# Kernel tuning notes

Hardware: AMD Instinct MI355X
Metric: run time of the kernel (lower is better)

## Reference

```python
import jax, jax.numpy as jnp
import numpy as np

TAU_EPS = 1e-6
T_SCALAR = 1.0  # call() default t when given a single tensor
NUM_HEADS = 8


def setup_inputs() -> dict:
    key = jax.random.key(0)
    ks = jax.random.split(key, 12)
    B, T, dm = 4, 1024, 512
    ph, th = 64, 32  # phi hidden, tau hidden
    pd = 128         # 2 * depth (pairwise concat dim per head)

    def w(k, shape):
        return jax.random.normal(k, shape, jnp.float32) / jnp.sqrt(jnp.float32(shape[0]))

    return {
        "x": jax.random.normal(ks[0], (B, T, dm), jnp.float32),
        "Wq": w(ks[1], (dm, dm)), "bq": jnp.zeros((dm,), jnp.float32),
        "Wk": w(ks[2], (dm, dm)), "bk": jnp.zeros((dm,), jnp.float32),
        "Wv": w(ks[3], (dm, dm)), "bv": jnp.zeros((dm,), jnp.float32),
        "Wphi_in": w(ks[4], (pd, ph)), "bphi_in": jnp.zeros((ph,), jnp.float32),
        "Wphi_out": w(ks[5], (ph, 1)), "bphi_out": jnp.zeros((1,), jnp.float32),
        "Wta": w(ks[6], (pd, 1)), "bta": jnp.zeros((1,), jnp.float32),
        "Wtb": w(ks[7], (pd, 1)), "btb": jnp.zeros((1,), jnp.float32),
        "Wtau_in": w(ks[8], (pd, th)), "btau_in": jnp.zeros((th,), jnp.float32),
        "Wtau_out": w(ks[9], (th, 1)), "btau_out": jnp.zeros((1,), jnp.float32),
        "Wo": w(ks[10], (dm, dm)), "bo": jnp.zeros((dm,), jnp.float32),
    }


def _lan_forward(x, Wq, bq, Wk, bk, Wv, bv,
                 Wphi_in, bphi_in, Wphi_out, bphi_out,
                 Wta, bta, Wtb, btb,
                 Wtau_in, btau_in, Wtau_out, btau_out,
                 Wo, bo):
    B, T, dm = x.shape
    H = NUM_HEADS
    D = dm // H

    def heads(z):  # [B,T,dm] -> [B,H,T,D]
        return z.reshape(B, T, H, D).transpose(0, 2, 1, 3)

    q = heads(x @ Wq + bq)
    k = heads(x @ Wk + bk)
    v = heads(x @ Wv + bv)

    # phi_in/phi_out, tau_in/tau_out, time_a, time_b are all linear Dense
    # layers acting on concat([q_i, k_j]) (dim 2D). A linear map on a concat
    # equals (per-q scalar) + (per-k scalar) + bias, so fold the two-layer
    # linear stacks into a single [2D] vector and broadcast-add -- exact math,
    # no [B,H,T,T,2D] materialization.
    def pair_scalar(w2d, b0):  # w2d: [2D], b0: scalar -> [B,H,Tq,Tk]
        sq = jnp.einsum('bhtd,d->bht', q, w2d[:D])
        sk = jnp.einsum('bhtd,d->bht', k, w2d[D:])
        return sq[..., :, None] + sk[..., None, :] + b0

    w_phi = (Wphi_in @ Wphi_out)[:, 0]
    b_phi = bphi_in @ Wphi_out[:, 0] + bphi_out[0]
    phi = jax.nn.sigmoid(pair_scalar(w_phi, b_phi))

    t_a = pair_scalar(Wta[:, 0], bta[0])
    t_b = pair_scalar(Wtb[:, 0], btb[0])
    t_interp = jax.nn.sigmoid(t_a * T_SCALAR + t_b)

    w_tau = (Wtau_in @ Wtau_out)[:, 0]
    b_tau = btau_in @ Wtau_out[:, 0] + btau_out[0]
    tau = jax.nn.softplus(pair_scalar(w_tau, b_tau)) + TAU_EPS

    # mode == 'exact': a(t) = (phi/tau) * (1 - exp(-tau * t))
    attn_logits = phi / tau * (1.0 - jnp.exp(-tau * t_interp))
    attn = jax.nn.softmax(attn_logits, axis=-1)

    out = jnp.einsum('bhqk,bhkd->bhqd', attn, v)          # [B,H,T,D]
    out = out.transpose(0, 2, 1, 3).reshape(B, T, dm)      # combine heads
    return out @ Wo + bo                                   # return_sequences=True, linear activation


def reference(x, Wq, bq, Wk, bk, Wv, bv,
              Wphi_in, bphi_in, Wphi_out, bphi_out,
              Wta, bta, Wtb, btb,
              Wtau_in, btau_in, Wtau_out, btau_out,
              Wo, bo):
    return _lan_forward(x, Wq, bq, Wk, bk, Wv, bv,
                        Wphi_in, bphi_in, Wphi_out, bphi_out,
                        Wta, bta, Wtb, btb,
                        Wtau_in, btau_in, Wtau_out, btau_out,
                        Wo, bo)
```

## Files before the change

### kernel.cpp

```cpp
#include <hip/hip_runtime.h>
#include <hip/hip_bf16.h>

#define B_  4
#define T_  1024
#define H_  8
#define NTOK (B_*T_)

#define CONST_OFF 512
#define UTH_OFF   576
#define UTL_OFF   12864
#define XHI_OFF   25152
#define WVTH_OFF  2122304
#define WOTH_OFF  2384448
#define S_OFF     2646592
#define VT_OFF    2843200

#define LOG2E 1.4426950408889634f
#define LN2SQ 0.4804530139182014f

typedef __attribute__((ext_vector_type(4))) float v4f;
typedef __attribute__((ext_vector_type(8))) short v8s;

__device__ inline short bf16r(float f) {
  union { float f; unsigned u; } v; v.f = f;
  return (short)((v.u + 0x7FFFu + ((v.u >> 16) & 1u)) >> 16);
}
__device__ inline float bf16f(short s) {
  union { unsigned u; float f; } v; v.u = ((unsigned)(unsigned short)s) << 16; return v.f;
}
__device__ inline unsigned cvt_pk_bf16(float lo, float hi) {
  unsigned r;
  asm("v_cvt_pk_bf16_f32 %0, %1, %2" : "=v"(r) : "v"(lo), "v"(hi));
  return r;
}

__global__ __launch_bounds__(256) void k_prep(
    const float* __restrict__ Wphi_in, const float* __restrict__ Wphi_out,
    const float* __restrict__ bphi_in, const float* __restrict__ bphi_out,
    const float* __restrict__ Wta, const float* __restrict__ bta,
    const float* __restrict__ Wtb, const float* __restrict__ btb,
    const float* __restrict__ Wtau_in, const float* __restrict__ Wtau_out,
    const float* __restrict__ btau_in, const float* __restrict__ btau_out,
    const float* __restrict__ Wq, const float* __restrict__ bq,
    const float* __restrict__ Wk, const float* __restrict__ bk,
    const float* __restrict__ x, const float* __restrict__ Wv, const float* __restrict__ Wo,
    short* __restrict__ Uth, short* __restrict__ Utl, float* __restrict__ consts,
    short* __restrict__ xh,
    short* __restrict__ Wvh, short* __restrict__ Woh) {
  __shared__ float wv[390];
  __shared__ float tile[64][65];
  int bx = blockIdx.x, t = threadIdx.x;
  if (bx < 96) {
    if (t < 128) {
      float wp = 0.f;
      for (int j = 0; j < 64; ++j) wp += Wphi_in[t*64+j] * Wphi_out[j];
      float wt = 0.f;
      for (int j = 0; j < 32; ++j) wt += Wtau_in[t*32+j] * Wtau_out[j];
      wv[t]       = wp;
      wv[128 + t] = Wta[t] + Wtb[t];
      wv[256 + t] = wt;
    } else if (t == 128) {
      float bp = bphi_out[0];
      for (int j = 0; j < 64; ++j) bp += bphi_in[j]*Wphi_out[j];
      float bt = btau_out[0];
      for (int j = 0; j < 32; ++j) bt += btau_in[j]*Wtau_out[j];
      wv[384] = bp;
      wv[385] = bta[0] + btb[0];
      wv[386] = bt;
    }
    __syncthreads();
    int idx = bx*256 + t;
    int c = idx & 511;
    int s = idx >> 9;
    int h = s / 6, tt = s % 6;
    int qk = tt / 3;
    int which = tt % 3;
    float scale = (which == 2) ? LOG2E : -LOG2E;
    const float* W = qk ? Wk : Wq;
    const float* wvec = wv + which*128 + qk*64;
    const float* row = W + c*512 + h*64;
    float acc = 0.f;
    #pragma unroll 8
    for (int d = 0; d < 64; ++d) acc += row[d] * wvec[d];
    float v = acc * scale;
    short hi = bf16r(v);
    Uth[s*512 + c] = hi;
    Utl[s*512 + c] = bf16r(v - bf16f(hi));
    if (c == 0) {
      const float* bb = qk ? bk : bq;
      float cs = 0.f;
      for (int d = 0; d < 64; ++d) cs += bb[h*64+d] * wvec[d];
      if (qk == 0) cs += wv[384 + which];
      consts[s] = cs * scale;
    }
    return;
  }
  if (bx < 1120) {
    size_t i = (size_t)((bx-96)*256 + t) * 8;
    float4 a = *(const float4*)(x + i);
    float4 b = *(const float4*)(x + i + 4);
    float vals[8] = {a.x,a.y,a.z,a.w,b.x,b.y,b.z,b.w};
    v8s hi;
    #pragma unroll
    for (int j = 0; j < 8; ++j) hi[j] = bf16r(vals[j]);
    *(v8s*)(xh + i) = hi;
    return;
  }
  int idx = bx - 1120;
  int z = idx >> 6, rem = idx & 63;
  int k0 = (rem >> 3)*64, n0 = (rem & 7)*64;
  const float* src = z ? Wo : Wv;
  short* dh = z ? Woh : Wvh;
  int kr = t >> 2, cq = t & 3;
  #pragma unroll
  for (int i = 0; i < 4; ++i) {
    float4 v = *(const float4*)(src + (size_t)(k0+kr)*512 + n0 + cq*16 + i*4);
    tile[kr][cq*16+i*4+0] = v.x; tile[kr][cq*16+i*4+1] = v.y;
    tile[kr][cq*16+i*4+2] = v.z; tile[kr][cq*16+i*4+3] = v.w;
  }
  __syncthreads();
  int nr = t >> 2, ko = t & 3;
  v8s h0,h1;
  #pragma unroll
  for (int i = 0; i < 8; ++i) {
    h0[i] = bf16r(tile[ko*16+i][nr]);
    h1[i] = bf16r(tile[ko*16+8+i][nr]);
  }
  size_t base = (size_t)(n0+nr)*512 + k0 + ko*16;
  *(v8s*)(dh + base) = h0; *(v8s*)(dh + base + 8) = h1;
}

template<int MODE>
__device__ __forceinline__ void gemm_body(char* smem, int mb, int nb,
    const short* __restrict__ A, const short* __restrict__ B,
    const float* __restrict__ bias, float* __restrict__ C, short* __restrict__ VT) {
  short (*As)[40] = (short(*)[40])(smem);
  short (*Bs)[40] = (short(*)[40])(smem + 5120);
  int tid = threadIdx.x, l = tid & 63, ra = l & 15, kg = l >> 4;
  int w = tid >> 6, wr = w >> 1, wc = w & 1;
  v4f acc[2][2] = {};
  int srow = tid >> 2, soct = tid & 3;
  const short* gA = A + (size_t)(mb*64+srow)*512 + soct*8;
  const short* gB = B + (size_t)(nb*64+srow)*512 + soct*8;
  v8s sa = *(const v8s*)(gA);
  v8s sc = *(const v8s*)(gB);
  for (int k0 = 0; k0 < 512; k0 += 32) {
    __syncthreads();
    *(v8s*)&As[srow][soct*8] = sa;
    *(v8s*)&Bs[srow][soct*8] = sc;
    if (k0 < 480) {
      sa = *(const v8s*)(gA + k0 + 32);
      sc = *(const v8s*)(gB + k0 + 32);
    }
    __syncthreads();
    v8s a[2], b[2];
    #pragma unroll
    for (int mi = 0; mi < 2; ++mi)
      a[mi] = *(const v8s*)&As[wr*32 + mi*16 + ra][kg*8];
    #pragma unroll
    for (int ni = 0; ni < 2; ++ni)
      b[ni] = *(const v8s*)&Bs[wc*32 + ni*16 + ra][kg*8];
    #pragma unroll
    for (int mi = 0; mi < 2; ++mi)
      #pragma unroll
      for (int ni = 0; ni < 2; ++ni)
        acc[mi][ni] = __builtin_amdgcn_mfma_f32_16x16x32_bf16(a[mi], b[ni], acc[mi][ni], 0, 0, 0);
  }
  if constexpr (MODE == 0) {
    #pragma unroll
    for (int ni = 0; ni < 2; ++ni) {
      int n = nb*64 + wc*32 + ni*16 + ra;
      float bv_ = bias[n];
      #pragma unroll
      for (int mi = 0; mi < 2; ++mi) {
        int row = mb*64 + wr*32 + mi*16 + kg*4;
        #pragma unroll
        for (int r = 0; r < 4; ++r)
          C[(size_t)(row+r)*512 + n] = acc[mi][ni][r] + bv_;
      }
    }
  } else {
    __syncthreads();
    float (*ldsT)[65] = (float(*)[65])(smem);
    #pragma unroll
    for (int ni = 0; ni < 2; ++ni) {
      int lc = wc*32 + ni*16 + ra;
      float bv_ = bias[nb*64 + lc];
      #pragma unroll
      for (int mi = 0; mi < 2; ++mi) {
        int lr = wr*32 + mi*16 + kg*4;
        #pragma unroll
        for (int r = 0; r < 4; ++r)
          ldsT[lc][lr+r] = acc[mi][ni][r] + bv_;
      }
    }
    __syncthreads();
    int d = tid >> 2, tq = tid & 3;
    v8s h0, h1;
    #pragma unroll
    for (int i = 0; i < 8; ++i) {
      h0[i] = bf16r(ldsT[d][tq*16+i]);
      h1[i] = bf16r(ldsT[d][tq*16+8+i]);
    }
    size_t base = ((size_t)(((mb>>4)*8 + nb)*64 + d))*1024 + (mb&15)*64 + tq*16;
    *(v8s*)(VT + base)     = h0;
    *(v8s*)(VT + base + 8) = h1;
  }
}

__device__ __forceinline__ void S_body(char* smem, int mb,
    const short* __restrict__ xh,
    const short* __restrict__ Uth, const short* __restrict__ Utl,
    const float* __restrict__ consts, float* __restrict__ E) {
  float* red = (float*)smem;
  int tid = threadIdx.x, w = tid >> 6, l = tid & 63, ra = l & 15, kg = l >> 4;
  v4f acc[3] = {{0,0,0,0},{0,0,0,0},{0,0,0,0}};
  const short* xa = xh + (size_t)(mb*16+ra)*512;
  #pragma unroll
  for (int ks = 0; ks < 4; ++ks) {
    int kk = w*128 + ks*32 + kg*8;
    v8s ah = *(const v8s*)(xa + kk);
    #pragma unroll
    for (int nf = 0; nf < 3; ++nf) {
      v8s bh = *(const v8s*)(Uth + (size_t)(nf*16+ra)*512 + kk);
      v8s bl = *(const v8s*)(Utl + (size_t)(nf*16+ra)*512 + kk);
      acc[nf] = __builtin_amdgcn_mfma_f32_16x16x32_bf16(ah, bh, acc[nf], 0, 0, 0);
      acc[nf] = __builtin_amdgcn_mfma_f32_16x16x32_bf16(ah, bl, acc[nf], 0, 0, 0);
    }
  }
  if (w > 0) {
    #pragma unroll
    for (int nf = 0; nf < 3; ++nf) *(v4f*)(red + ((w-1)*64 + l)*12 + nf*4) = acc[nf];
  }
  __syncthreads();
  if (w == 0) {
    #pragma unroll
    for (int p = 0; p < 3; ++p)
      #pragma unroll
      for (int nf = 0; nf < 3; ++nf) acc[nf] += *(const v4f*)(red + (p*64 + l)*12 + nf*4);
    int t0 = mb*16 + kg*4;
    #pragma unroll
    for (int nf = 0; nf < 3; ++nf) {
      int s = nf*16 + ra;
      float cns = consts[s];
      v4f o;
      #pragma unroll
      for (int c = 0; c < 4; ++c) o[c] = __builtin_amdgcn_exp2f(acc[nf][c] + cns);
      *(v4f*)(E + (size_t)s*NTOK + t0) = o;
    }
  }
}

__global__ __launch_bounds__(256) void k_mid(
    const short* __restrict__ xh,
    const short* __restrict__ Uth, const short* __restrict__ Utl,
    const float* __restrict__ consts, float* __restrict__ E,
    const short* __restrict__ Wvh,
    const float* __restrict__ bv, short* __restrict__ VT) {
  __shared__ __align__(16) char smem[16640];
  int bx = blockIdx.x;
  if (bx < 256) {
    S_body(smem, bx, xh, Uth, Utl, consts, E);
  } else {
    int i = bx - 256;
    gemm_body<1>(smem, i >> 3, i & 7, xh, Wvh, bv, nullptr, VT);
  }
}

__global__ __launch_bounds__(256) void k_out(
    const short* __restrict__ A, const short* __restrict__ B,
    const float* __restrict__ bias, float* __restrict__ C) {
  __shared__ __align__(16) char smem[16640];
  gemm_body<0>(smem, blockIdx.x, blockIdx.y, A, B, bias, C, nullptr);
}

__global__ __launch_bounds__(256) void k_attn(const float* __restrict__ E,
                                              const short* __restrict__ VT,
                                              short* __restrict__ AOh) {
  __shared__ float red[3][64][40];
  int tid = threadIdx.x, w = tid >> 6, l = tid & 63, ra = l & 15, kg = l >> 4;
  int bh = blockIdx.y, b = bh >> 3, h = bh & 7;
  int q0 = blockIdx.x * 32;
  const float* Eb = E + (size_t)h*6*NTOK + b*T_;
  float eqp[2], eqc[2], eqt[2];
  #pragma unroll
  for (int ai = 0; ai < 2; ++ai) {
    eqp[ai] = Eb[q0 + ai*16 + ra];
    eqc[ai] = Eb[NTOK + q0 + ai*16 + ra];
    eqt[ai] = Eb[2*NTOK + q0 + ai*16 + ra];
  }
  const float* Ekp = Eb + 3*NTOK;
  const float* Ekc = Eb + 4*NTOK;
  const float* Ekt = Eb + 5*NTOK;
  const short* Vb = VT + (size_t)bh*64*1024 + (size_t)ra*1024;

  v4f acc[2][4] = {};
  v4f dacc[2] = {};
  v8s ones;
  #pragma unroll
  for (int j = 0; j < 8; ++j) ones[j] = (short)0x3F80;

  #pragma unroll 2
  for (int ks = 0; ks < 8; ++ks) {
    int kk = w*256 + ks*32 + kg*8;
    v4f p0 = *(const v4f*)&Ekp[kk], p1 = *(const v4f*)&Ekp[kk+4];
    v4f c0 = *(const v4f*)&Ekc[kk], c1 = *(const v4f*)&Ekc[kk+4];
    v4f t0 = *(const v4f*)&Ekt[kk], t1 = *(const v4f*)&Ekt[kk+4];
    v8s bfr[4];
    #pragma unroll
    for (int ni = 0; ni < 4; ++ni) bfr[ni] = *(const v8s*)(Vb + (size_t)ni*16*1024 + kk);
    #pragma unroll
    for (int ai = 0; ai < 2; ++ai) {
      float p8[8];
      #pragma unroll
      for (int j = 0; j < 8; ++j) {
        float Ep = (j < 4) ? p0[j] : p1[j-4];
        float Ec = (j < 4) ? c0[j] : c1[j-4];
        float Et = (j < 4) ? t0[j] : t1[j-4];
        float ephi = eqp[ai] * Ep;
        float ec   = eqc[ai] * Ec;
        float g    = eqt[ai] * Et;
        float ti   = __builtin_amdgcn_rcpf(1.f + ec);
        float t2   = __builtin_amdgcn_logf(1.f + g);
        float z    = 1.f - __builtin_amdgcn_exp2f(-t2 * ti);
        float den  = (1.f + ephi) * fmaf(t2, LN2SQ, 6.93e-7f);
        p8[j] = __builtin_amdgcn_exp2f(z * __builtin_amdgcn_rcpf(den));
      }
      union { unsigned u[4]; v8s s; } af;
      af.u[0] = cvt_pk_bf16(p8[0], p8[1]);
      af.u[1] = cvt_pk_bf16(p8[2], p8[3]);
      af.u[2] = cvt_pk_bf16(p8[4], p8[5]);
      af.u[3] = cvt_pk_bf16(p8[6], p8[7]);
      v8s afrag = af.s;
      #pragma unroll
      for (int ni = 0; ni < 4; ++ni)
        acc[ai][ni] = __builtin_amdgcn_mfma_f32_16x16x32_bf16(afrag, bfr[ni], acc[ai][ni], 0, 0, 0);
      dacc[ai] = __builtin_amdgcn_mfma_f32_16x16x32_bf16(afrag, ones, dacc[ai], 0, 0, 0);
    }
  }

  if (w > 0) {
    float* rp = &red[w-1][l][0];
    #pragma unroll
    for (int ai = 0; ai < 2; ++ai) {
      #pragma unroll
      for (int ni = 0; ni < 4; ++ni) *(v4f*)(rp + ai*16 + ni*4) = acc[ai][ni];
      *(v4f*)(rp + 32 + ai*4) = dacc[ai];
    }
  }
  __syncthreads();
  if (w == 0) {
    #pragma unroll
    for (int p = 0; p < 3; ++p) {
      const float* rp = &red[p][l][0];
      #pragma unroll
      for (int ai = 0; ai < 2; ++ai) {
        #pragma unroll
        for (int ni = 0; ni < 4; ++ni) acc[ai][ni] += *(const v4f*)(rp + ai*16 + ni*4);
        dacc[ai] += *(const v4f*)(rp + 32 + ai*4);
      }
    }
    #pragma unroll
    for (int ai = 0; ai < 2; ++ai) {
      size_t qb = (size_t)(b*T_ + q0 + ai*16 + kg*4);
      #pragma unroll
      for (int r = 0; r < 4; ++r) {
        float inv = __builtin_amdgcn_rcpf(dacc[ai][r]);
        size_t o = (qb + r)*512 + h*64 + ra;
        #pragma unroll
        for (int ni = 0; ni < 4; ++ni)
          AOh[o + ni*16] = bf16r(acc[ai][ni][r] * inv);
      }
    }
  }
}

extern "C" void kernel_launch(void* const* d_in, const int* in_sizes, int n_in,
                              void* d_out, int out_size, void* d_ws, size_t ws_size,
                              hipStream_t stream) {
  (void)in_sizes; (void)n_in; (void)out_size; (void)ws_size;
  const float* x        = (const float*)d_in[0];
  const float* Wq       = (const float*)d_in[1];
  const float* bq       = (const float*)d_in[2];
  const float* Wk       = (const float*)d_in[3];
  const float* bk       = (const float*)d_in[4];
  const float* Wv       = (const float*)d_in[5];
  const float* bv       = (const float*)d_in[6];
  const float* Wphi_in  = (const float*)d_in[7];
  const float* bphi_in  = (const float*)d_in[8];
  const float* Wphi_out = (const float*)d_in[9];
  const float* bphi_out = (const float*)d_in[10];
  const float* Wta      = (const float*)d_in[11];
  const float* bta      = (const float*)d_in[12];
  const float* Wtb      = (const float*)d_in[13];
  const float* btb      = (const float*)d_in[14];
  const float* Wtau_in  = (const float*)d_in[15];
  const float* btau_in  = (const float*)d_in[16];
  const float* Wtau_out = (const float*)d_in[17];
  const float* btau_out = (const float*)d_in[18];
  const float* Wo       = (const float*)d_in[19];
  const float* bo       = (const float*)d_in[20];
  float* out = (float*)d_out;
  float* ws  = (float*)d_ws;

  float* consts = ws + CONST_OFF;
  short* Uth    = (short*)(ws + UTH_OFF);
  short* Utl    = (short*)(ws + UTL_OFF);
  short* xhi    = (short*)(ws + XHI_OFF);
  short* AOh    = (short*)(ws + XHI_OFF);
  short* Wvth   = (short*)(ws + WVTH_OFF);
  short* Woth   = (short*)(ws + WOTH_OFF);
  float* E      = ws + S_OFF;
  short* VT     = (short*)(ws + VT_OFF);

  hipLaunchKernelGGL(k_prep, dim3(1248), dim3(256), 0, stream,
                     Wphi_in, Wphi_out, bphi_in, bphi_out, Wta, bta, Wtb, btb,
                     Wtau_in, Wtau_out, btau_in, btau_out,
                     Wq, bq, Wk, bk, x, Wv, Wo,
                     Uth, Utl, consts, xhi, Wvth, Woth);
  hipLaunchKernelGGL(k_mid, dim3(768), dim3(256), 0, stream,
                     xhi, Uth, Utl, consts, E, Wvth, bv, VT);
  hipLaunchKernelGGL(k_attn, dim3(T_/32, B_*H_), dim3(256), 0, stream, E, VT, AOh);
  hipLaunchKernelGGL(k_out, dim3(NTOK/64, 8), dim3(256), 0, stream,
                     AOh, Woth, bo, out);
}
```

Baseline: 57.27 us.

## Double-buffer GEMM LDS tiles and replace attention exp2 with polynomial

The GEMM body now alternates between two LDS buffers, which removes one of the two barriers per k-step, and LDS use grows to 20 KB. In the attention inner loop the products plus one become fmaf, and the log scaling moves from ln2^2 to ln2 so the argument is in natural-log units. The final exp2 (transcendental unit) is replaced by a degree-5 Taylor polynomial for exp(u), trading one transcendental for several FMAs. The polynomial is only accurate for small |u|, so results could drift if the logits are large, though bf16 rounding of the probabilities may hide some of that error.

New measurement: 65.07 us. 13.6% more time.

```diff
diff --git a/kernel.cpp b/kernel.cpp
--- a/kernel.cpp
+++ b/kernel.cpp
@@ -16,7 +16,7 @@
 #define VT_OFF    2843200
 
 #define LOG2E 1.4426950408889634f
-#define LN2SQ 0.4804530139182014f
+#define LN2   0.6931471805599453f
 
 typedef __attribute__((ext_vector_type(4))) float v4f;
 typedef __attribute__((ext_vector_type(8))) short v8s;
@@ -134,8 +134,6 @@
 __device__ __forceinline__ void gemm_body(char* smem, int mb, int nb,
     const short* __restrict__ A, const short* __restrict__ B,
     const float* __restrict__ bias, float* __restrict__ C, short* __restrict__ VT) {
-  short (*As)[40] = (short(*)[40])(smem);
-  short (*Bs)[40] = (short(*)[40])(smem + 5120);
   int tid = threadIdx.x, l = tid & 63, ra = l & 15, kg = l >> 4;
   int w = tid >> 6, wr = w >> 1, wc = w & 1;
   v4f acc[2][2] = {};
@@ -144,13 +142,16 @@
   const short* gB = B + (size_t)(nb*64+srow)*512 + soct*8;
   v8s sa = *(const v8s*)(gA);
   v8s sc = *(const v8s*)(gB);
-  for (int k0 = 0; k0 < 512; k0 += 32) {
-    __syncthreads();
+  #pragma unroll 2
+  for (int t = 0; t < 16; ++t) {
+    char* buf = smem + (t & 1)*10240;
+    short (*As)[40] = (short(*)[40])(buf);
+    short (*Bs)[40] = (short(*)[40])(buf + 5120);
     *(v8s*)&As[srow][soct*8] = sa;
     *(v8s*)&Bs[srow][soct*8] = sc;
-    if (k0 < 480) {
-      sa = *(const v8s*)(gA + k0 + 32);
-      sc = *(const v8s*)(gB + k0 + 32);
+    if (t < 15) {
+      sa = *(const v8s*)(gA + (t+1)*32);
+      sc = *(const v8s*)(gB + (t+1)*32);
     }
     __syncthreads();
     v8s a[2], b[2];
@@ -257,7 +258,7 @@
     const float* __restrict__ consts, float* __restrict__ E,
     const short* __restrict__ Wvh,
     const float* __restrict__ bv, short* __restrict__ VT) {
-  __shared__ __align__(16) char smem[16640];
+  __shared__ __align__(16) char smem[20480];
   int bx = blockIdx.x;
   if (bx < 256) {
     S_body(smem, bx, xh, Uth, Utl, consts, E);
@@ -270,7 +271,7 @@
 __global__ __launch_bounds__(256) void k_out(
     const short* __restrict__ A, const short* __restrict__ B,
     const float* __restrict__ bias, float* __restrict__ C) {
-  __shared__ __align__(16) char smem[16640];
+  __shared__ __align__(16) char smem[20480];
   gemm_body<0>(smem, blockIdx.x, blockIdx.y, A, B, bias, C, nullptr);
 }
 
@@ -317,14 +318,21 @@
         float Ep = (j < 4) ? p0[j] : p1[j-4];
         float Ec = (j < 4) ? c0[j] : c1[j-4];
         float Et = (j < 4) ? t0[j] : t1[j-4];
-        float ephi = eqp[ai] * Ep;
-        float ec   = eqc[ai] * Ec;
-        float g    = eqt[ai] * Et;
-        float ti   = __builtin_amdgcn_rcpf(1.f + ec);
-        float t2   = __builtin_amdgcn_logf(1.f + g);
-        float z    = 1.f - __builtin_amdgcn_exp2f(-t2 * ti);
-        float den  = (1.f + ephi) * fmaf(t2, LN2SQ, 6.93e-7f);
-        p8[j] = __builtin_amdgcn_exp2f(z * __builtin_amdgcn_rcpf(den));
+        float aphi = fmaf(eqp[ai], Ep, 1.f);
+        float a1   = fmaf(eqc[ai], Ec, 1.f);
+        float ag   = fmaf(eqt[ai], Et, 1.f);
+        float ti   = __builtin_amdgcn_rcpf(a1);
+        float t2   = __builtin_amdgcn_logf(ag);
+        float q_   = __builtin_amdgcn_exp2f(-t2 * ti);
+        float den  = aphi * fmaf(t2, LN2, 1e-6f);
+        float rd   = __builtin_amdgcn_rcpf(den);
+        float u    = (1.f - q_) * rd;
+        float p    = fmaf(u, 8.3333333e-3f, 4.1666667e-2f);
+        p = fmaf(u, p, 0.16666667f);
+        p = fmaf(u, p, 0.5f);
+        p = fmaf(u, p, 1.f);
+        p = fmaf(u, p, 1.f);
+        p8[j] = p;
       }
       union { unsigned u[4]; v8s s; } af;
       af.u[0] = cvt_pk_bf16(p8[0], p8[1]);
```
